# Optimization experiments

Measured on AMD Instinct MI355X. Metric: run time of the kernel, lower is better.

Reference implementation:

```python
import jax, jax.numpy as jnp
import numpy as np

M, K, N = 8192, 4096, 4096

def setup_inputs() -> dict:
    key = jax.random.key(0)
    k0, k1, k2, k3, k4 = jax.random.split(key, 5)
    x = jax.random.normal(k0, (M, K), dtype=jnp.float32)
    # int8 weight stored as int32 spec dtype; values in [-127, 127]
    weight = jax.random.randint(k1, (N, K), -127, 128, dtype=jnp.int32)
    input_scale = jnp.array([0.02], dtype=jnp.float32)
    input_offset = jnp.zeros((1,), dtype=jnp.int32)
    # per-output-channel dequant scale (small positive)
    deq_scale = jax.random.uniform(k2, (N,), dtype=jnp.float32, minval=1e-4, maxval=2e-4)
    quant_bias = jax.random.randint(k3, (N,), -100, 101, dtype=jnp.int32)
    # sparse-compression output-channel reorder index (a permutation)
    index = jax.random.permutation(k4, N).astype(jnp.int32)
    return {"x": x, "weight": weight, "input_scale": input_scale,
            "input_offset": input_offset, "deq_scale": deq_scale,
            "quant_bias": quant_bias, "index": index}

def reference(x, weight, input_scale, input_offset, deq_scale, quant_bias, index):
    # 1) per-tensor activation quantization to int8
    x_q = jnp.clip(jnp.round(x / input_scale) + input_offset.astype(jnp.float32),
                   -128.0, 127.0).astype(jnp.int8)
    acc = jnp.matmul(x_q.astype(jnp.int32), weight.astype(jnp.int8).astype(jnp.int32).T)
    acc = acc + quant_bias  # [M, N] int32
    # 3) per-channel dequantization
    y = acc.astype(jnp.float32) * deq_scale  # [M, N]
    # 4) restore output-channel order from compressed layout
    return jnp.take(y, index, axis=-1)
```

## Files before the change

kernel.cpp:

```cpp
#include <hip/hip_runtime.h>
#include <hip/hip_bf16.h>
#include <stdint.h>

#define M_DIM 8192
#define K_DIM 4096
#define N_DIM 4096

#define BM 256
#define BN 256
#define BKB 64
#define NT (K_DIM / BKB)
#define ATILE (BM * BKB)
#define TBYTES (ATILE + BN * BKB)

typedef int i32x4 __attribute__((ext_vector_type(4)));

__global__ __launch_bounds__(256) void quant_x_kernel(
    const float* __restrict__ x, const float* __restrict__ scale_p,
    const int* __restrict__ off_p, int8_t* __restrict__ xq)
{
    const float s = scale_p[0];
    const float off = (float)off_p[0];
    long base = ((long)blockIdx.x * 256 + threadIdx.x) * 16;
    const float4* xin = (const float4*)(x + base);
    float v[16];
    *(float4*)(v + 0)  = xin[0];
    *(float4*)(v + 4)  = xin[1];
    *(float4*)(v + 8)  = xin[2];
    *(float4*)(v + 12) = xin[3];
    uint32_t pk[4];
#pragma unroll
    for (int g = 0; g < 4; ++g) {
        uint32_t p = 0;
#pragma unroll
        for (int j = 0; j < 4; ++j) {
            float q = rintf(v[g * 4 + j] / s) + off;
            q = fminf(fmaxf(q, -128.0f), 127.0f);
            int qi = (int)q;
            p |= ((uint32_t)(qi & 0xff)) << (8 * j);
        }
        pk[g] = p;
    }
    uint4 o; o.x = pk[0]; o.y = pk[1]; o.z = pk[2]; o.w = pk[3];
    *(uint4*)(xq + base) = o;
}

__global__ __launch_bounds__(256) void pack_w_kernel(
    const int* __restrict__ w, const int* __restrict__ index,
    const float* __restrict__ deq, const int* __restrict__ qb,
    int8_t* __restrict__ bp, float* __restrict__ dsp, int* __restrict__ qbp)
{
    int j = blockIdx.x;
    int t = threadIdx.x;
    int src = index[j];
    const int4* wrow = (const int4*)(w + (long)src * K_DIM);
    uint32_t pk[4];
#pragma unroll
    for (int g = 0; g < 4; ++g) {
        int4 c = wrow[t * 4 + g];
        pk[g] = ((uint32_t)(c.x & 0xff)) | (((uint32_t)(c.y & 0xff)) << 8) |
                (((uint32_t)(c.z & 0xff)) << 16) | (((uint32_t)(c.w & 0xff)) << 24);
    }
    uint4 o; o.x = pk[0]; o.y = pk[1]; o.z = pk[2]; o.w = pk[3];
    *(uint4*)(bp + (long)j * K_DIM + t * 16) = o;
    if (t == 0) { dsp[j] = deq[src]; qbp[j] = qb[src]; }
}

__device__ __forceinline__ void gload_lds16(const int8_t* g, int8_t* l)
{
    __builtin_amdgcn_global_load_lds(
        (const __attribute__((address_space(1))) uint32_t*)g,
        (__attribute__((address_space(3))) uint32_t*)l, 16, 0, 0);
}

__global__ __launch_bounds__(512, 2) void gemm_i8_kernel(
    const int8_t* __restrict__ A, const int8_t* __restrict__ B,
    const float* __restrict__ dsp, const int* __restrict__ qbp,
    float* __restrict__ C)
{
    __shared__ int8_t tb0[TBYTES];
    __shared__ int8_t tb1[TBYTES];
    __shared__ int8_t tb2[TBYTES];

    int bid = blockIdx.x;
    int swz = (bid & 7) * (gridDim.x >> 3) + (bid >> 3);
    int bm = swz & 31;
    int bn = swz >> 5;
    int brow = bm * BM, bcol = bn * BN;

    int t = threadIdx.x;
    int wv = t >> 6;
    int l  = t & 63;
    int lr = l & 15;
    int ls = l >> 4;
    int wrM = (wv >> 2) * 128;
    int wcN = (wv & 3) * 64;
    int pslot = ls ^ ((lr >> 1) & 3);

    int aoff[8], boff[4];
#pragma unroll
    for (int m = 0; m < 8; ++m)
        aoff[m] = (wrM + m * 16 + lr) * BKB + pslot * 16;
#pragma unroll
    for (int n = 0; n < 4; ++n)
        boff[n] = ATILE + (wcN + n * 16 + lr) * BKB + pslot * 16;

    int ca0 = t, ca1 = 512 + t;
    int r0 = ca0 >> 2, r1 = ca1 >> 2;
    const int8_t* sa0 = A + (long)(brow + r0) * K_DIM + ((ca0 & 3) ^ ((r0 >> 1) & 3)) * 16;
    const int8_t* sa1 = A + (long)(brow + r1) * K_DIM + ((ca1 & 3) ^ ((r1 >> 1) & 3)) * 16;
    const int8_t* sb0 = B + (long)(bcol + r0) * K_DIM + ((ca0 & 3) ^ ((r0 >> 1) & 3)) * 16;
    const int8_t* sb1 = B + (long)(bcol + r1) * K_DIM + ((ca1 & 3) ^ ((r1 >> 1) & 3)) * 16;
    const int da0 = ca0 * 16, da1 = ca1 * 16;
    const int db0 = ATILE + ca0 * 16, db1 = ATILE + ca1 * 16;

#define STAGE4(STG) do { \
        gload_lds16(sa0, (STG) + da0); \
        gload_lds16(sa1, (STG) + da1); \
        gload_lds16(sb0, (STG) + db0); \
        gload_lds16(sb1, (STG) + db1); \
        sa0 += BKB; sa1 += BKB; sb0 += BKB; sb1 += BKB; \
    } while (0)

#define GEMM_TILE(CUR, STG, KT) do { \
        i32x4 af[8], bf[4]; \
        _Pragma("unroll") \
        for (int n = 0; n < 4; ++n) bf[n] = *(const i32x4*)((CUR) + boff[n]); \
        _Pragma("unroll") \
        for (int m = 0; m < 8; ++m) af[m] = *(const i32x4*)((CUR) + aoff[m]); \
        const bool _st = (KT) + 2 < NT; \
        if (_st) STAGE4(STG); \
        _Pragma("unroll") \
        for (int m = 0; m < 8; ++m) \
        _Pragma("unroll") \
        for (int n = 0; n < 4; ++n) \
            acc[m][n] = __builtin_amdgcn_mfma_i32_16x16x64_i8( \
                af[m], bf[n], acc[m][n], 0, 0, 0); \
        asm volatile("s_waitcnt lgkmcnt(0)" ::: "memory"); \
        if (_st) asm volatile("s_waitcnt vmcnt(4)" ::: "memory"); \
        else     asm volatile("s_waitcnt vmcnt(0)" ::: "memory"); \
        __builtin_amdgcn_s_barrier(); \
    } while (0)

    STAGE4(tb0);
    STAGE4(tb1);
    asm volatile("s_waitcnt vmcnt(4)" ::: "memory");
    __builtin_amdgcn_s_barrier();

    i32x4 acc[8][4] = {};

    for (int kt = 0; kt < 63; kt += 3) {
        GEMM_TILE(tb0, tb2, kt);
        GEMM_TILE(tb1, tb0, kt + 1);
        GEMM_TILE(tb2, tb1, kt + 2);
    }
    {
        i32x4 af[8], bf[4];
#pragma unroll
        for (int n = 0; n < 4; ++n) bf[n] = *(const i32x4*)(tb0 + boff[n]);
#pragma unroll
        for (int m = 0; m < 8; ++m) af[m] = *(const i32x4*)(tb0 + aoff[m]);
#pragma unroll
        for (int m = 0; m < 8; ++m)
#pragma unroll
            for (int n = 0; n < 4; ++n)
                acc[m][n] = __builtin_amdgcn_mfma_i32_16x16x64_i8(
                    af[m], bf[n], acc[m][n], 0, 0, 0);
    }

#undef STAGE4
#undef GEMM_TILE

#pragma unroll
    for (int n = 0; n < 4; ++n) {
        int gc = bcol + wcN + n * 16 + lr;
        float ds = dsp[gc];
        int qb = qbp[gc];
#pragma unroll
        for (int m = 0; m < 8; ++m) {
            int gr0 = brow + wrM + m * 16 + ls * 4;
#pragma unroll
            for (int r = 0; r < 4; ++r) {
                C[(long)(gr0 + r) * N_DIM + gc] = (float)(acc[m][n][r] + qb) * ds;
            }
        }
    }
}

extern "C" void kernel_launch(void* const* d_in, const int* in_sizes, int n_in,
                              void* d_out, int out_size, void* d_ws, size_t ws_size,
                              hipStream_t stream)
{
    (void)in_sizes; (void)n_in; (void)out_size; (void)ws_size;
    const float* x   = (const float*)d_in[0];
    const int*   w   = (const int*)d_in[1];
    const float* is  = (const float*)d_in[2];
    const int*   io  = (const int*)d_in[3];
    const float* dq  = (const float*)d_in[4];
    const int*   qb  = (const int*)d_in[5];
    const int*   idx = (const int*)d_in[6];
    float* out = (float*)d_out;

    int8_t* xq  = (int8_t*)d_ws;
    int8_t* bp  = xq + (size_t)M_DIM * K_DIM;
    float*  dsp = (float*)(bp + (size_t)N_DIM * K_DIM);
    int*    qbp = (int*)(dsp + N_DIM);

    long quant_blocks = ((long)M_DIM * K_DIM) / 16 / 256;
    quant_x_kernel<<<(int)quant_blocks, 256, 0, stream>>>(x, is, io, xq);
    pack_w_kernel<<<N_DIM, 256, 0, stream>>>(w, idx, dq, qb, bp, dsp, qbp);
    gemm_i8_kernel<<<(M_DIM / BM) * (N_DIM / BN), 512, 0, stream>>>(xq, bp, dsp, qbp, out);
}
```

Baseline: 197.5 us.

## Restructure int8 GEMM to 4 waves with 128x128 warp tiles and BK=128 double buffering

Switches the GEMM block from 8 waves to 4, giving each wave a 128x128 output tile (8x8 MFMA accumulators) for more register-level reuse of LDS fragments. The K tile doubles to 128 bytes with a new 8-way XOR swizzle, and the three-stage LDS ring becomes a two-buffer scheme that waits for all global loads (vmcnt(0)) before each barrier. This halves the number of barriers and raises the MFMA-to-LDS-read ratio. In exchange it needs 256 accumulator registers per lane, runs at occupancy 1, and loses the deeper prefetch overlap.

Result: slower. 259.6 us (+31.4%).

```diff
diff --git a/kernel.cpp b/kernel.cpp
--- a/kernel.cpp
+++ b/kernel.cpp
@@ -8,10 +8,10 @@
 
 #define BM 256
 #define BN 256
-#define BKB 64
+#define BKB 128
 #define NT (K_DIM / BKB)
 #define ATILE (BM * BKB)
-#define TBYTES (ATILE + BN * BKB)
+#define TBYTES (2 * ATILE)
 
 typedef int i32x4 __attribute__((ext_vector_type(4)));
 
@@ -73,14 +73,13 @@
         (__attribute__((address_space(3))) uint32_t*)l, 16, 0, 0);
 }
 
-__global__ __launch_bounds__(512, 2) void gemm_i8_kernel(
+__global__ __launch_bounds__(256, 1) void gemm_i8_kernel(
     const int8_t* __restrict__ A, const int8_t* __restrict__ B,
     const float* __restrict__ dsp, const int* __restrict__ qbp,
     float* __restrict__ C)
 {
     __shared__ int8_t tb0[TBYTES];
     __shared__ int8_t tb1[TBYTES];
-    __shared__ int8_t tb2[TBYTES];
 
     int bid = blockIdx.x;
     int swz = (bid & 7) * (gridDim.x >> 3) + (bid >> 3);
@@ -93,86 +92,79 @@
     int l  = t & 63;
     int lr = l & 15;
     int ls = l >> 4;
-    int wrM = (wv >> 2) * 128;
-    int wcN = (wv & 3) * 64;
-    int pslot = ls ^ ((lr >> 1) & 3);
-
-    int aoff[8], boff[4];
-#pragma unroll
-    for (int m = 0; m < 8; ++m)
-        aoff[m] = (wrM + m * 16 + lr) * BKB + pslot * 16;
-#pragma unroll
-    for (int n = 0; n < 4; ++n)
-        boff[n] = ATILE + (wcN + n * 16 + lr) * BKB + pslot * 16;
-
-    int ca0 = t, ca1 = 512 + t;
-    int r0 = ca0 >> 2, r1 = ca1 >> 2;
-    const int8_t* sa0 = A + (long)(brow + r0) * K_DIM + ((ca0 & 3) ^ ((r0 >> 1) & 3)) * 16;
-    const int8_t* sa1 = A + (long)(brow + r1) * K_DIM + ((ca1 & 3) ^ ((r1 >> 1) & 3)) * 16;
-    const int8_t* sb0 = B + (long)(bcol + r0) * K_DIM + ((ca0 & 3) ^ ((r0 >> 1) & 3)) * 16;
-    const int8_t* sb1 = B + (long)(bcol + r1) * K_DIM + ((ca1 & 3) ^ ((r1 >> 1) & 3)) * 16;
-    const int da0 = ca0 * 16, da1 = ca1 * 16;
-    const int db0 = ATILE + ca0 * 16, db1 = ATILE + ca1 * 16;
-
-#define STAGE4(STG) do { \
-        gload_lds16(sa0, (STG) + da0); \
-        gload_lds16(sa1, (STG) + da1); \
-        gload_lds16(sb0, (STG) + db0); \
-        gload_lds16(sb1, (STG) + db1); \
-        sa0 += BKB; sa1 += BKB; sb0 += BKB; sb1 += BKB; \
+    int wrM = (wv >> 1) * 128;
+    int wcN = (wv & 1) * 128;
+    int p0 = ls ^ (lr & 7);
+
+    const int aL0 = (wrM + lr) * BKB + p0 * 16;
+    const int bL0 = ATILE + (wcN + lr) * BKB + p0 * 16;
+    const int aL1 = aL0 ^ 64;
+    const int bL1 = bL0 ^ 64;
+
+    int rowl = t >> 3;
+    int lg = (t & 7) ^ (rowl & 7);
+    const int8_t* sA = A + (long)(brow + rowl) * K_DIM + lg * 16;
+    const int8_t* sB = B + (long)(bcol + rowl) * K_DIM + lg * 16;
+    const int dal = t * 16;
+
+#define STAGE16(STG) do { \
+        _Pragma("unroll") \
+        for (int i = 0; i < 8; ++i) \
+            gload_lds16(sA + (long)i * (32 * K_DIM), (STG) + i * 4096 + dal); \
+        _Pragma("unroll") \
+        for (int i = 0; i < 8; ++i) \
+            gload_lds16(sB + (long)i * (32 * K_DIM), (STG) + ATILE + i * 4096 + dal); \
+        sA += BKB; sB += BKB; \
     } while (0)
 
-#define GEMM_TILE(CUR, STG, KT) do { \
-        i32x4 af[8], bf[4]; \
-        _Pragma("unroll") \
-        for (int n = 0; n < 4; ++n) bf[n] = *(const i32x4*)((CUR) + boff[n]); \
-        _Pragma("unroll") \
-        for (int m = 0; m < 8; ++m) af[m] = *(const i32x4*)((CUR) + aoff[m]); \
-        const bool _st = (KT) + 2 < NT; \
-        if (_st) STAGE4(STG); \
+#define TILE(CUR, STG, DO_STAGE, LAST) do { \
+        i32x4 af[8], bf[8], af2[8], bf2[8]; \
+        _Pragma("unroll") \
+        for (int n = 0; n < 8; ++n) bf[n] = *(const i32x4*)((CUR) + bL0 + n * 2048); \
+        _Pragma("unroll") \
+        for (int m = 0; m < 8; ++m) af[m] = *(const i32x4*)((CUR) + aL0 + m * 2048); \
         _Pragma("unroll") \
         for (int m = 0; m < 8; ++m) \
         _Pragma("unroll") \
-        for (int n = 0; n < 4; ++n) \
+        for (int n = 0; n < 8; ++n) \
             acc[m][n] = __builtin_amdgcn_mfma_i32_16x16x64_i8( \
                 af[m], bf[n], acc[m][n], 0, 0, 0); \
-        asm volatile("s_waitcnt lgkmcnt(0)" ::: "memory"); \
-        if (_st) asm volatile("s_waitcnt vmcnt(4)" ::: "memory"); \
-        else     asm volatile("s_waitcnt vmcnt(0)" ::: "memory"); \
-        __builtin_amdgcn_s_barrier(); \
+        _Pragma("unroll") \
+        for (int n = 0; n < 8; ++n) bf2[n] = *(const i32x4*)((CUR) + bL1 + n * 2048); \
+        _Pragma("unroll") \
+        for (int m = 0; m < 8; ++m) af2[m] = *(const i32x4*)((CUR) + aL1 + m * 2048); \
+        if (DO_STAGE) STAGE16(STG); \
+        _Pragma("unroll") \
+        for (int m = 0; m < 8; ++m) \
+        _Pragma("unroll") \
+        for (int n = 0; n < 8; ++n) \
+            acc[m][n] = __builtin_amdgcn_mfma_i32_16x16x64_i8( \
+                af2[m], bf2[n], acc[m][n], 0, 0, 0); \
+        if (!(LAST)) { \
+            asm volatile("s_waitcnt lgkmcnt(0)" ::: "memory"); \
+            asm volatile("s_waitcnt vmcnt(0)" ::: "memory"); \
+            __builtin_amdgcn_s_barrier(); \
+        } \
     } while (0)
 
-    STAGE4(tb0);
-    STAGE4(tb1);
-    asm volatile("s_waitcnt vmcnt(4)" ::: "memory");
+    STAGE16(tb0);
+    asm volatile("s_waitcnt vmcnt(0)" ::: "memory");
     __builtin_amdgcn_s_barrier();
 
-    i32x4 acc[8][4] = {};
-
-    for (int kt = 0; kt < 63; kt += 3) {
-        GEMM_TILE(tb0, tb2, kt);
-        GEMM_TILE(tb1, tb0, kt + 1);
-        GEMM_TILE(tb2, tb1, kt + 2);
-    }
-    {
-        i32x4 af[8], bf[4];
-#pragma unroll
-        for (int n = 0; n < 4; ++n) bf[n] = *(const i32x4*)(tb0 + boff[n]);
-#pragma unroll
-        for (int m = 0; m < 8; ++m) af[m] = *(const i32x4*)(tb0 + aoff[m]);
-#pragma unroll
-        for (int m = 0; m < 8; ++m)
-#pragma unroll
-            for (int n = 0; n < 4; ++n)
-                acc[m][n] = __builtin_amdgcn_mfma_i32_16x16x64_i8(
-                    af[m], bf[n], acc[m][n], 0, 0, 0);
-    }
-
-#undef STAGE4
-#undef GEMM_TILE
-
-#pragma unroll
-    for (int n = 0; n < 4; ++n) {
+    i32x4 acc[8][8] = {};
+
+    for (int it = 0; it < 15; ++it) {
+        TILE(tb0, tb1, true, false);
+        TILE(tb1, tb0, true, false);
+    }
+    TILE(tb0, tb1, true, false);
+    TILE(tb1, tb0, false, true);
+
+#undef STAGE16
+#undef TILE
+
+#pragma unroll
+    for (int n = 0; n < 8; ++n) {
         int gc = bcol + wcN + n * 16 + lr;
         float ds = dsp[gc];
         int qb = qbp[gc];
@@ -209,5 +201,5 @@
     long quant_blocks = ((long)M_DIM * K_DIM) / 16 / 256;
     quant_x_kernel<<<(int)quant_blocks, 256, 0, stream>>>(x, is, io, xq);
     pack_w_kernel<<<N_DIM, 256, 0, stream>>>(w, idx, dq, qb, bp, dsp, qbp);
-    gemm_i8_kernel<<<(M_DIM / BM) * (N_DIM / BN), 512, 0, stream>>>(xq, bp, dsp, qbp, out);
-}
+    gemm_i8_kernel<<<(M_DIM / BM) * (N_DIM / BN), 256, 0, stream>>>(xq, bp, dsp, qbp, out);
+}
```

## Use a 4-stage LDS ring with register double-buffered fragments interleaved with MFMA

Applied to the files above, without the earlier changes.

The int8 GEMM main loop moves from a 3-buffer LDS ring to a 4-buffer ring, so staging runs three tiles ahead. A/B fragments are now double-buffered in registers: the next tile's LDS reads and global-to-LDS copies are split into four groups, each interleaved with a quarter of the current tile's MFMAs. The interleaving is pinned with sched_barrier and setprio. This aims to hide LDS read latency and global load issue behind matrix math. The cost is 128KB of LDS per block, more fragment registers and a longer epilogue.

Result: slower. 214.9 us (+8.8%).

```diff
diff --git a/kernel.cpp b/kernel.cpp
--- a/kernel.cpp
+++ b/kernel.cpp
@@ -81,6 +81,7 @@
     __shared__ int8_t tb0[TBYTES];
     __shared__ int8_t tb1[TBYTES];
     __shared__ int8_t tb2[TBYTES];
+    __shared__ int8_t tb3[TBYTES];
 
     int bid = blockIdx.x;
     int swz = (bid & 7) * (gridDim.x >> 3) + (bid >> 3);
@@ -114,6 +115,57 @@
     const int da0 = ca0 * 16, da1 = ca1 * 16;
     const int db0 = ATILE + ca0 * 16, db1 = ATILE + ca1 * 16;
 
+    i32x4 afA[8], bfA[4], afB[8], bfB[4];
+    i32x4 acc[8][4] = {};
+
+#define MF2(AFR, BFR, M0) do { \
+        _Pragma("unroll") \
+        for (int mm = 0; mm < 2; ++mm) \
+        _Pragma("unroll") \
+        for (int nn = 0; nn < 4; ++nn) \
+            acc[(M0) + mm][nn] = __builtin_amdgcn_mfma_i32_16x16x64_i8( \
+                AFR[(M0) + mm], BFR[nn], acc[(M0) + mm][nn], 0, 0, 0); \
+    } while (0)
+
+#define SB0() __builtin_amdgcn_sched_barrier(0)
+
+#define TILE(AFR, BFR, AFW, BFW, RD, STG, DO_ST, VMC) do { \
+         \
+        if (DO_ST) { gload_lds16(sa0, (STG) + da0); sa0 += BKB; } \
+        BFW[0] = *(const i32x4*)((RD) + boff[0]); \
+        BFW[1] = *(const i32x4*)((RD) + boff[1]); \
+        BFW[2] = *(const i32x4*)((RD) + boff[2]); \
+        SB0(); __builtin_amdgcn_s_setprio(1); \
+        MF2(AFR, BFR, 0); \
+        __builtin_amdgcn_s_setprio(0); SB0(); \
+         \
+        if (DO_ST) { gload_lds16(sa1, (STG) + da1); sa1 += BKB; } \
+        BFW[3] = *(const i32x4*)((RD) + boff[3]); \
+        AFW[0] = *(const i32x4*)((RD) + aoff[0]); \
+        AFW[1] = *(const i32x4*)((RD) + aoff[1]); \
+        SB0(); __builtin_amdgcn_s_setprio(1); \
+        MF2(AFR, BFR, 2); \
+        __builtin_amdgcn_s_setprio(0); SB0(); \
+         \
+        if (DO_ST) { gload_lds16(sb0, (STG) + db0); sb0 += BKB; } \
+        AFW[2] = *(const i32x4*)((RD) + aoff[2]); \
+        AFW[3] = *(const i32x4*)((RD) + aoff[3]); \
+        AFW[4] = *(const i32x4*)((RD) + aoff[4]); \
+        SB0(); __builtin_amdgcn_s_setprio(1); \
+        MF2(AFR, BFR, 4); \
+        __builtin_amdgcn_s_setprio(0); SB0(); \
+         \
+        if (DO_ST) { gload_lds16(sb1, (STG) + db1); sb1 += BKB; } \
+        AFW[5] = *(const i32x4*)((RD) + aoff[5]); \
+        AFW[6] = *(const i32x4*)((RD) + aoff[6]); \
+        AFW[7] = *(const i32x4*)((RD) + aoff[7]); \
+        SB0(); __builtin_amdgcn_s_setprio(1); \
+        MF2(AFR, BFR, 6); \
+        __builtin_amdgcn_s_setprio(0); SB0(); \
+        asm volatile("s_waitcnt vmcnt(" #VMC ")" ::: "memory"); \
+        __builtin_amdgcn_s_barrier(); \
+    } while (0)
+
 #define STAGE4(STG) do { \
         gload_lds16(sa0, (STG) + da0); \
         gload_lds16(sa1, (STG) + da1); \
@@ -122,54 +174,46 @@
         sa0 += BKB; sa1 += BKB; sb0 += BKB; sb1 += BKB; \
     } while (0)
 
-#define GEMM_TILE(CUR, STG, KT) do { \
-        i32x4 af[8], bf[4]; \
-        _Pragma("unroll") \
-        for (int n = 0; n < 4; ++n) bf[n] = *(const i32x4*)((CUR) + boff[n]); \
-        _Pragma("unroll") \
-        for (int m = 0; m < 8; ++m) af[m] = *(const i32x4*)((CUR) + aoff[m]); \
-        const bool _st = (KT) + 2 < NT; \
-        if (_st) STAGE4(STG); \
-        _Pragma("unroll") \
-        for (int m = 0; m < 8; ++m) \
-        _Pragma("unroll") \
-        for (int n = 0; n < 4; ++n) \
-            acc[m][n] = __builtin_amdgcn_mfma_i32_16x16x64_i8( \
-                af[m], bf[n], acc[m][n], 0, 0, 0); \
-        asm volatile("s_waitcnt lgkmcnt(0)" ::: "memory"); \
-        if (_st) asm volatile("s_waitcnt vmcnt(4)" ::: "memory"); \
-        else     asm volatile("s_waitcnt vmcnt(0)" ::: "memory"); \
-        __builtin_amdgcn_s_barrier(); \
-    } while (0)
-
-    STAGE4(tb0);
-    STAGE4(tb1);
+    STAGE4(tb0); STAGE4(tb1); STAGE4(tb2);
     asm volatile("s_waitcnt vmcnt(4)" ::: "memory");
     __builtin_amdgcn_s_barrier();
 
-    i32x4 acc[8][4] = {};
-
-    for (int kt = 0; kt < 63; kt += 3) {
-        GEMM_TILE(tb0, tb2, kt);
-        GEMM_TILE(tb1, tb0, kt + 1);
-        GEMM_TILE(tb2, tb1, kt + 2);
-    }
+#pragma unroll
+    for (int n = 0; n < 4; ++n) bfA[n] = *(const i32x4*)(tb0 + boff[n]);
+#pragma unroll
+    for (int m = 0; m < 8; ++m) afA[m] = *(const i32x4*)(tb0 + aoff[m]);
+
+    for (int it = 0; it < 15; ++it) {
+        TILE(afA, bfA, afB, bfB, tb1, tb3, true, 4);
+        TILE(afB, bfB, afA, bfA, tb2, tb0, true, 4);
+        TILE(afA, bfA, afB, bfB, tb3, tb1, true, 4);
+        TILE(afB, bfB, afA, bfA, tb0, tb2, true, 4);
+    }
+    TILE(afA, bfA, afB, bfB, tb1, tb3, true, 4);
+    TILE(afB, bfB, afA, bfA, tb2, tb0, false, 0);
     {
-        i32x4 af[8], bf[4];
-#pragma unroll
-        for (int n = 0; n < 4; ++n) bf[n] = *(const i32x4*)(tb0 + boff[n]);
-#pragma unroll
-        for (int m = 0; m < 8; ++m) af[m] = *(const i32x4*)(tb0 + aoff[m]);
+#pragma unroll
+        for (int n = 0; n < 4; ++n) bfB[n] = *(const i32x4*)(tb3 + boff[n]);
+#pragma unroll
+        for (int m = 0; m < 8; ++m) afB[m] = *(const i32x4*)(tb3 + aoff[m]);
 #pragma unroll
         for (int m = 0; m < 8; ++m)
 #pragma unroll
             for (int n = 0; n < 4; ++n)
                 acc[m][n] = __builtin_amdgcn_mfma_i32_16x16x64_i8(
-                    af[m], bf[n], acc[m][n], 0, 0, 0);
-    }
-
+                    afA[m], bfA[n], acc[m][n], 0, 0, 0);
+    }
+#pragma unroll
+    for (int m = 0; m < 8; ++m)
+#pragma unroll
+        for (int n = 0; n < 4; ++n)
+            acc[m][n] = __builtin_amdgcn_mfma_i32_16x16x64_i8(
+                afB[m], bfB[n], acc[m][n], 0, 0, 0);
+
+#undef TILE
 #undef STAGE4
-#undef GEMM_TILE
+#undef MF2
+#undef SB0
 
 #pragma unroll
     for (int n = 0; n < 4; ++n) {
```

## Switch int8 GEMM to 32x32x32 MFMA tiles and remap block ordering

Applied to the files above, without the earlier changes.

Replaces the 16x16x64 int8 MFMA micro-tiles with 32x32x32 int8 MFMA, reorganising per-wave fragments into 4x2 tiles that each take two K-halves, with matching LDS offsets and epilogue row mapping. The larger MFMA shape cuts LDS fragment reads per FLOP and the instruction count. It also changes the swizzled block-to-tile mapping so consecutive blocks walk along N instead of M, which alters L2 reuse. Each accumulator is now 16 registers wide, so register pressure may change.

Result: no change. 198.0 us (+0.3%).

```diff
diff --git a/kernel.cpp b/kernel.cpp
--- a/kernel.cpp
+++ b/kernel.cpp
@@ -13,7 +13,8 @@
 #define ATILE (BM * BKB)
 #define TBYTES (ATILE + BN * BKB)
 
-typedef int i32x4 __attribute__((ext_vector_type(4)));
+typedef int i32x4  __attribute__((ext_vector_type(4)));
+typedef int i32x16 __attribute__((ext_vector_type(16)));
 
 __global__ __launch_bounds__(256) void quant_x_kernel(
     const float* __restrict__ x, const float* __restrict__ scale_p,
@@ -84,26 +85,34 @@
 
     int bid = blockIdx.x;
     int swz = (bid & 7) * (gridDim.x >> 3) + (bid >> 3);
-    int bm = swz & 31;
-    int bn = swz >> 5;
+    int bn = swz & 15;
+    int bm = swz >> 4;
     int brow = bm * BM, bcol = bn * BN;
 
     int t = threadIdx.x;
     int wv = t >> 6;
     int l  = t & 63;
-    int lr = l & 15;
-    int ls = l >> 4;
+    int r32 = l & 31;
+    int kh  = l >> 5;
     int wrM = (wv >> 2) * 128;
     int wcN = (wv & 3) * 64;
-    int pslot = ls ^ ((lr >> 1) & 3);
-
-    int aoff[8], boff[4];
-#pragma unroll
-    for (int m = 0; m < 8; ++m)
-        aoff[m] = (wrM + m * 16 + lr) * BKB + pslot * 16;
-#pragma unroll
-    for (int n = 0; n < 4; ++n)
-        boff[n] = ATILE + (wcN + n * 16 + lr) * BKB + pslot * 16;
+    int sxor = (r32 >> 1) & 3;
+
+    int aoff[4][2], boff[2][2];
+#pragma unroll
+    for (int m = 0; m < 4; ++m)
+#pragma unroll
+        for (int kk = 0; kk < 2; ++kk) {
+            int s = kk * 2 + kh;
+            aoff[m][kk] = (wrM + m * 32 + r32) * BKB + (s ^ sxor) * 16;
+        }
+#pragma unroll
+    for (int n = 0; n < 2; ++n)
+#pragma unroll
+        for (int kk = 0; kk < 2; ++kk) {
+            int s = kk * 2 + kh;
+            boff[n][kk] = ATILE + (wcN + n * 32 + r32) * BKB + (s ^ sxor) * 16;
+        }
 
     int ca0 = t, ca1 = 512 + t;
     int r0 = ca0 >> 2, r1 = ca1 >> 2;
@@ -123,19 +132,25 @@
     } while (0)
 
 #define GEMM_TILE(CUR, STG, KT) do { \
-        i32x4 af[8], bf[4]; \
-        _Pragma("unroll") \
-        for (int n = 0; n < 4; ++n) bf[n] = *(const i32x4*)((CUR) + boff[n]); \
-        _Pragma("unroll") \
-        for (int m = 0; m < 8; ++m) af[m] = *(const i32x4*)((CUR) + aoff[m]); \
+        i32x4 af[4][2], bf[2][2]; \
+        _Pragma("unroll") \
+        for (int n = 0; n < 2; ++n) bf[n][0] = *(const i32x4*)((CUR) + boff[n][0]); \
+        _Pragma("unroll") \
+        for (int m = 0; m < 4; ++m) af[m][0] = *(const i32x4*)((CUR) + aoff[m][0]); \
+        _Pragma("unroll") \
+        for (int n = 0; n < 2; ++n) bf[n][1] = *(const i32x4*)((CUR) + boff[n][1]); \
+        _Pragma("unroll") \
+        for (int m = 0; m < 4; ++m) af[m][1] = *(const i32x4*)((CUR) + aoff[m][1]); \
         const bool _st = (KT) + 2 < NT; \
         if (_st) STAGE4(STG); \
         _Pragma("unroll") \
-        for (int m = 0; m < 8; ++m) \
-        _Pragma("unroll") \
-        for (int n = 0; n < 4; ++n) \
-            acc[m][n] = __builtin_amdgcn_mfma_i32_16x16x64_i8( \
-                af[m], bf[n], acc[m][n], 0, 0, 0); \
+        for (int kk = 0; kk < 2; ++kk) \
+        _Pragma("unroll") \
+        for (int m = 0; m < 4; ++m) \
+        _Pragma("unroll") \
+        for (int n = 0; n < 2; ++n) \
+            acc[m][n] = __builtin_amdgcn_mfma_i32_32x32x32_i8( \
+                af[m][kk], bf[n][kk], acc[m][n], 0, 0, 0); \
         asm volatile("s_waitcnt lgkmcnt(0)" ::: "memory"); \
         if (_st) asm volatile("s_waitcnt vmcnt(4)" ::: "memory"); \
         else     asm volatile("s_waitcnt vmcnt(0)" ::: "memory"); \
@@ -147,7 +162,7 @@
     asm volatile("s_waitcnt vmcnt(4)" ::: "memory");
     __builtin_amdgcn_s_barrier();
 
-    i32x4 acc[8][4] = {};
+    i32x16 acc[4][2] = {};
 
     for (int kt = 0; kt < 63; kt += 3) {
         GEMM_TILE(tb0, tb2, kt);
@@ -155,33 +170,38 @@
         GEMM_TILE(tb2, tb1, kt + 2);
     }
     {
-        i32x4 af[8], bf[4];
-#pragma unroll
-        for (int n = 0; n < 4; ++n) bf[n] = *(const i32x4*)(tb0 + boff[n]);
-#pragma unroll
-        for (int m = 0; m < 8; ++m) af[m] = *(const i32x4*)(tb0 + aoff[m]);
-#pragma unroll
-        for (int m = 0; m < 8; ++m)
-#pragma unroll
-            for (int n = 0; n < 4; ++n)
-                acc[m][n] = __builtin_amdgcn_mfma_i32_16x16x64_i8(
-                    af[m], bf[n], acc[m][n], 0, 0, 0);
+        i32x4 af[4][2], bf[2][2];
+#pragma unroll
+        for (int n = 0; n < 2; ++n) { bf[n][0] = *(const i32x4*)(tb0 + boff[n][0]);
+                                      bf[n][1] = *(const i32x4*)(tb0 + boff[n][1]); }
+#pragma unroll
+        for (int m = 0; m < 4; ++m) { af[m][0] = *(const i32x4*)(tb0 + aoff[m][0]);
+                                      af[m][1] = *(const i32x4*)(tb0 + aoff[m][1]); }
+#pragma unroll
+        for (int kk = 0; kk < 2; ++kk)
+#pragma unroll
+        for (int m = 0; m < 4; ++m)
+#pragma unroll
+        for (int n = 0; n < 2; ++n)
+            acc[m][n] = __builtin_amdgcn_mfma_i32_32x32x32_i8(
+                af[m][kk], bf[n][kk], acc[m][n], 0, 0, 0);
     }
 
 #undef STAGE4
 #undef GEMM_TILE
 
 #pragma unroll
-    for (int n = 0; n < 4; ++n) {
-        int gc = bcol + wcN + n * 16 + lr;
+    for (int n = 0; n < 2; ++n) {
+        int gc = bcol + wcN + n * 32 + r32;
         float ds = dsp[gc];
         int qb = qbp[gc];
 #pragma unroll
-        for (int m = 0; m < 8; ++m) {
-            int gr0 = brow + wrM + m * 16 + ls * 4;
-#pragma unroll
-            for (int r = 0; r < 4; ++r) {
-                C[(long)(gr0 + r) * N_DIM + gc] = (float)(acc[m][n][r] + qb) * ds;
+        for (int m = 0; m < 4; ++m) {
+            int grb = brow + wrM + m * 32 + 4 * kh;
+#pragma unroll
+            for (int q = 0; q < 16; ++q) {
+                int gr = grb + (q & 3) + 8 * (q >> 2);
+                C[(long)gr * N_DIM + gc] = (float)(acc[m][n][q] + qb) * ds;
             }
         }
     }
```
